# Performance work log

Measured on AMD Instinct MI355X. Metric: run time of the kernel, lower is better.

Reference implementation:

```python
import jax, jax.numpy as jnp
import numpy as np

BLOCK = 64  # bnb 4-bit quant block size along the input dim

def dequant4bit(q, scale):
    # q: [out, in] int codes in [0,16); scale: [out, in//BLOCK]
    # symmetric 4-bit dequant: w = (code - 7.5) * blockwise scale
    return (q.astype(jnp.float32) - 7.5) * jnp.repeat(scale, BLOCK, axis=1)

def setup_inputs() -> dict:
    key = jax.random.key(0)
    ks = jax.random.split(key, 11)
    B, S, D, H, R = 4, 2048, 2048, 8192, 16
    return {
        "x1": jax.random.normal(ks[0], (B, S, D), jnp.float32),
        "w_up_q": jax.random.randint(ks[1], (H, D), 0, 16, dtype=jnp.int32),
        "w_up_scale": jax.random.uniform(ks[2], (H, D // BLOCK), jnp.float32) * 0.02,
        "b_up": jax.random.normal(ks[3], (H,), jnp.float32) * 0.01,
        "w_up_lora_a": jax.random.normal(ks[4], (D, R), jnp.float32) * 0.02,
        "w_up_lora_b": jax.random.normal(ks[5], (R, H), jnp.float32) * 0.02,
        "w_down_q": jax.random.randint(ks[6], (D, H), 0, 16, dtype=jnp.int32),
        "w_down_scale": jax.random.uniform(ks[7], (D, H // BLOCK), jnp.float32) * 0.02,
        "b_down": jax.random.normal(ks[8], (D,), jnp.float32) * 0.01,
        "w_down_lora_a": jax.random.normal(ks[9], (H, R), jnp.float32) * 0.02,
        "w_down_lora_b": jax.random.normal(ks[10], (R, D), jnp.float32) * 0.02,
    }

def reference(x1, w_up_q, w_up_scale, b_up, w_up_lora_a, w_up_lora_b,
              w_down_q, w_down_scale, b_down, w_down_lora_a, w_down_lora_b):
    # up projection: dequant-matmul + bias + LoRA (activation_forward='relu')
    w_up = dequant4bit(w_up_q, w_up_scale).T            # [D, H]
    y1 = x1 @ w_up + b_up + (x1 @ w_up_lora_a) @ w_up_lora_b   # [B, S, H]
    x2 = jax.nn.relu(y1)
    # down projection: dequant-matmul + bias + LoRA
    w_down = dequant4bit(w_down_q, w_down_scale).T      # [H, D]
    y2 = x2 @ w_down + b_down + (x2 @ w_down_lora_a) @ w_down_lora_b  # [B, S, D]
    return y2
```

## Files before the change

### kernel.cpp

```cpp
#include <hip/hip_runtime.h>
#include <hip/hip_bf16.h>
#include <stdint.h>
#include <stddef.h>

typedef __bf16 bf16;
typedef bf16  bf16x4 __attribute__((ext_vector_type(4)));
typedef bf16  bf16x8 __attribute__((ext_vector_type(8)));
typedef float f32x4  __attribute__((ext_vector_type(4)));

__device__ __forceinline__ void async_copy16(bf16* lds, const bf16* g) {
    __builtin_amdgcn_global_load_lds(
        (const __attribute__((address_space(1))) void*)g,
        (__attribute__((address_space(3))) void*)lds,
        16, 0, 0);
}

__device__ __forceinline__ void bar() { __builtin_amdgcn_s_barrier(); }
#define SFENCE() __builtin_amdgcn_sched_barrier(0)
#define WAIT_LGKM0() do { asm volatile("s_waitcnt lgkmcnt(0)"); SFENCE(); } while (0)
#define WAIT_VM6()   do { asm volatile("s_waitcnt vmcnt(6)");   SFENCE(); } while (0)
#define WAIT_VM0()   do { asm volatile("s_waitcnt vmcnt(0)");   SFENCE(); } while (0)

__global__ __launch_bounds__(256) void cast_f32_to_bf16(
        const float* __restrict__ in, bf16* __restrict__ out, int n4) {
    int i = blockIdx.x * blockDim.x + threadIdx.x;
    if (i >= n4) return;
    const float4 v = *(const float4*)(in + (size_t)i * 4);
    bf16x4 o;
    o[0] = (bf16)v.x; o[1] = (bf16)v.y; o[2] = (bf16)v.z; o[3] = (bf16)v.w;
    *(bf16x4*)(out + (size_t)i * 4) = o;
}

__global__ __launch_bounds__(256) void dequant_lora(
        const int*   __restrict__ q,
        const float* __restrict__ scale,
        const float* __restrict__ A,
        const float* __restrict__ Bm,
        bf16* __restrict__ out,
        int N, int K) {
    const int tid = threadIdx.x;
    const int k0 = blockIdx.x * 64;
    const int n0 = blockIdx.y * 64;
    const int kk = k0 + (tid & 15) * 4;
    const int nb = n0 + (tid >> 4) * 4;

    f32x4 Ar[4][4];
    #pragma unroll
    for (int i = 0; i < 4; ++i)
        #pragma unroll
        for (int rq = 0; rq < 4; ++rq)
            Ar[i][rq] = *(const f32x4*)&A[(size_t)(kk + i) * 16 + rq * 4];
    f32x4 Br[16];
    #pragma unroll
    for (int r = 0; r < 16; ++r)
        Br[r] = *(const f32x4*)&Bm[(size_t)r * N + nb];

    const int scol = (unsigned)k0 >> 6;
    #pragma unroll
    for (int nn = 0; nn < 4; ++nn) {
        const int n = nb + nn;
        const int4 qv = *(const int4*)&q[(size_t)n * K + kk];
        const float s = scale[(size_t)n * (K >> 6) + scol];
        float l0 = 0.f, l1 = 0.f, l2 = 0.f, l3 = 0.f;
        #pragma unroll
        for (int r = 0; r < 16; ++r) {
            const float bv = Br[r][nn];
            l0 += Ar[0][r >> 2][r & 3] * bv;
            l1 += Ar[1][r >> 2][r & 3] * bv;
            l2 += Ar[2][r >> 2][r & 3] * bv;
            l3 += Ar[3][r >> 2][r & 3] * bv;
        }
        bf16x4 o;
        o[0] = (bf16)(((float)qv.x - 7.5f) * s + l0);
        o[1] = (bf16)(((float)qv.y - 7.5f) * s + l1);
        o[2] = (bf16)(((float)qv.z - 7.5f) * s + l2);
        o[3] = (bf16)(((float)qv.w - 7.5f) * s + l3);
        *(bf16x4*)&out[(size_t)n * K + kk] = o;
    }
}

template <bool RELU, typename OUT_T>
__global__ __launch_bounds__(512, 2) void gemm_bt256(
        const bf16* __restrict__ A, const bf16* __restrict__ B,
        const float* __restrict__ bias, OUT_T* __restrict__ C,
        int M, int N, int K) {
    __shared__ __attribute__((aligned(16))) bf16 As[2][2][128 * 64];
    __shared__ __attribute__((aligned(16))) bf16 Bs[2][2][128 * 64];

    const int tid  = threadIdx.x;
    const int wave = tid >> 6;
    const int lane = tid & 63;
    const int wm   = wave >> 2;
    const int wn   = wave & 3;
    const int bn   = blockIdx.x;
    const int bm   = blockIdx.y;

    const int srow = tid >> 3;
    const int scol = ((tid & 7) ^ (srow & 7)) * 8;
    const bf16* gA = A + ((size_t)(bm * 256) + srow) * K + scol;
    const bf16* gB = B + ((size_t)(bn * 256) + srow) * K + scol;

    auto STAGE_A = [&](int h, int tt) {
        bf16* l = &As[tt & 1][h][wave * 512];
        const bf16* g = gA + (size_t)h * 128 * K + (size_t)tt * 64;
        async_copy16(l, g);
        async_copy16(l + 4096, g + (size_t)64 * K);
    };
    auto STAGE_B = [&](int h, int tt) {
        bf16* l = &Bs[tt & 1][h][wave * 512];
        const bf16* g = gB + (size_t)h * 128 * K + (size_t)tt * 64;
        async_copy16(l, g);
        async_copy16(l + 4096, g + (size_t)64 * K);
    };

    const int fr  = lane & 15;
    const int kq  = lane >> 4;
    const int cg0 = ((kq    ) ^ (fr & 7)) * 8;
    const int cg1 = ((kq + 4) ^ (fr & 7)) * 8;
    const int ra  = fr * 64;
    const int rb  = (wn & 1) * 4096 + fr * 64;

    f32x4 acc[8][4];
    #pragma unroll
    for (int i = 0; i < 8; ++i)
        #pragma unroll
        for (int j = 0; j < 4; ++j) {
            f32x4 z = {0.f, 0.f, 0.f, 0.f};
            acc[i][j] = z;
        }

    STAGE_B(0, 0); STAGE_B(1, 0); STAGE_A(0, 0); STAGE_A(1, 0);
    STAGE_B(0, 1); STAGE_B(1, 1); STAGE_A(0, 1);
    WAIT_VM6();
    bar();

    const int NT = K >> 6;
    bf16x8 fa[4][2], fb[4][2];

    for (int t = 0; t < NT; ++t) {
        const int p = t & 1;
        const bf16* aH = &As[p][wm][0];
        const bf16* bH = &Bs[p][wn >> 1][0];

        #pragma unroll
        for (int i = 0; i < 4; ++i) {
            fa[i][0] = *(const bf16x8*)(aH + i * 1024 + ra + cg0);
            fa[i][1] = *(const bf16x8*)(aH + i * 1024 + ra + cg1);
        }
        #pragma unroll
        for (int j = 0; j < 4; ++j) {
            fb[j][0] = *(const bf16x8*)(bH + rb + j * 1024 + cg0);
            fb[j][1] = *(const bf16x8*)(bH + rb + j * 1024 + cg1);
        }
        if (t + 1 < NT) STAGE_A(1, t + 1);
        bar();
        WAIT_LGKM0();
        __builtin_amdgcn_s_setprio(1);
        #pragma unroll
        for (int ks = 0; ks < 2; ++ks)
            #pragma unroll
            for (int i = 0; i < 4; ++i)
                #pragma unroll
                for (int j = 0; j < 2; ++j)
                    acc[i][j] = __builtin_amdgcn_mfma_f32_16x16x32_bf16(
                        fa[i][ks], fb[j][ks], acc[i][j], 0, 0, 0);
        __builtin_amdgcn_s_setprio(0);
        bar();

        if (t + 2 < NT) STAGE_B(0, t + 2);
        bar();
        WAIT_LGKM0();
        __builtin_amdgcn_s_setprio(1);
        #pragma unroll
        for (int ks = 0; ks < 2; ++ks)
            #pragma unroll
            for (int i = 0; i < 4; ++i)
                #pragma unroll
                for (int j = 2; j < 4; ++j)
                    acc[i][j] = __builtin_amdgcn_mfma_f32_16x16x32_bf16(
                        fa[i][ks], fb[j][ks], acc[i][j], 0, 0, 0);
        __builtin_amdgcn_s_setprio(0);
        bar();

        #pragma unroll
        for (int i = 0; i < 4; ++i) {
            fa[i][0] = *(const bf16x8*)(aH + (i + 4) * 1024 + ra + cg0);
            fa[i][1] = *(const bf16x8*)(aH + (i + 4) * 1024 + ra + cg1);
        }
        if (t + 2 < NT) STAGE_B(1, t + 2);
        bar();
        WAIT_LGKM0();
        __builtin_amdgcn_s_setprio(1);
        #pragma unroll
        for (int ks = 0; ks < 2; ++ks)
            #pragma unroll
            for (int i = 0; i < 4; ++i)
                #pragma unroll
                for (int j = 2; j < 4; ++j)
                    acc[i + 4][j] = __builtin_amdgcn_mfma_f32_16x16x32_bf16(
                        fa[i][ks], fb[j][ks], acc[i + 4][j], 0, 0, 0);
        __builtin_amdgcn_s_setprio(0);
        bar();

        if (t + 2 < NT) {
            STAGE_A(0, t + 2);
            WAIT_VM6();
        } else {
            WAIT_VM0();
        }
        bar();
        __builtin_amdgcn_s_setprio(1);
        #pragma unroll
        for (int ks = 0; ks < 2; ++ks)
            #pragma unroll
            for (int i = 0; i < 4; ++i)
                #pragma unroll
                for (int j = 0; j < 2; ++j)
                    acc[i + 4][j] = __builtin_amdgcn_mfma_f32_16x16x32_bf16(
                        fa[i][ks], fb[j][ks], acc[i + 4][j], 0, 0, 0);
        __builtin_amdgcn_s_setprio(0);
        bar();
    }

    const int er = bm * 256 + wm * 128 + (lane >> 4) * 4;
    const int ec = bn * 256 + wn * 64 + fr;
    #pragma unroll
    for (int j = 0; j < 4; ++j) {
        const int col = ec + j * 16;
        const float bv = bias[col];
        #pragma unroll
        for (int i = 0; i < 8; ++i) {
            #pragma unroll
            for (int r = 0; r < 4; ++r) {
                const int row = er + i * 16 + r;
                float v = acc[i][j][r] + bv;
                if (RELU) v = v > 0.f ? v : 0.f;
                C[(size_t)row * N + col] = (OUT_T)v;
            }
        }
    }
}

extern "C" void kernel_launch(void* const* d_in, const int* in_sizes, int n_in,
                              void* d_out, int out_size, void* d_ws, size_t ws_size,
                              hipStream_t stream) {
    const float* x1           = (const float*)d_in[0];
    const int*   w_up_q       = (const int*)  d_in[1];
    const float* w_up_scale   = (const float*)d_in[2];
    const float* b_up         = (const float*)d_in[3];
    const float* w_up_lora_a  = (const float*)d_in[4];
    const float* w_up_lora_b  = (const float*)d_in[5];
    const int*   w_down_q     = (const int*)  d_in[6];
    const float* w_down_scale = (const float*)d_in[7];
    const float* b_down       = (const float*)d_in[8];
    const float* w_down_lora_a= (const float*)d_in[9];
    const float* w_down_lora_b= (const float*)d_in[10];
    float* out = (float*)d_out;

    const int M = 8192, D = 2048, H = 8192;

    char* ws = (char*)d_ws;
    bf16* x1b = (bf16*)ws;
    bf16* wup = (bf16*)(ws + (size_t)M * D * 2);
    bf16* x2  = (bf16*)(ws + (size_t)M * D * 2 + (size_t)H * D * 2);
    bf16* wdn = x1b;

    {
        int n4 = (M * D) / 4;
        cast_f32_to_bf16<<<dim3((n4 + 255) / 256), dim3(256), 0, stream>>>(x1, x1b, n4);
    }
    dequant_lora<<<dim3(D / 64, H / 64), dim3(256), 0, stream>>>(
        w_up_q, w_up_scale, w_up_lora_a, w_up_lora_b, wup, H, D);
    gemm_bt256<true, bf16><<<dim3(H / 256, M / 256), dim3(512), 0, stream>>>(
        x1b, wup, b_up, x2, M, H, D);
    dequant_lora<<<dim3(H / 64, D / 64), dim3(256), 0, stream>>>(
        w_down_q, w_down_scale, w_down_lora_a, w_down_lora_b, wdn, D, H);
    gemm_bt256<false, float><<<dim3(D / 256, M / 256), dim3(512), 0, stream>>>(
        x2, wdn, b_down, out, M, D, H);
}
```

Before: 784.3 us.

## Prefetch next A fragments into registers and unroll GEMM loop by two stages

Restructures the 256x256 bf16 GEMM main loop so the first half of the next tile's A fragments is loaded from LDS during the last MFMA phase of the current tile. The loop is unrolled by two, with the LDS buffers split into separate named arrays, so buffer selection is resolved at compile time. LDS waits are moved to after the MFMA blocks instead of before them, overlapping LDS reads with matrix math. This adds another set of fragment registers, which could cause spills at 2 blocks per CU, and assumes NT is even.

```diff
diff --git a/kernel.cpp b/kernel.cpp
--- a/kernel.cpp
+++ b/kernel.cpp
@@ -84,8 +84,10 @@
         const bf16* __restrict__ A, const bf16* __restrict__ B,
         const float* __restrict__ bias, OUT_T* __restrict__ C,
         int M, int N, int K) {
-    __shared__ __attribute__((aligned(16))) bf16 As[2][2][128 * 64];
-    __shared__ __attribute__((aligned(16))) bf16 Bs[2][2][128 * 64];
+    __shared__ __attribute__((aligned(16))) bf16 As0[2][8192];
+    __shared__ __attribute__((aligned(16))) bf16 As1[2][8192];
+    __shared__ __attribute__((aligned(16))) bf16 Bs0[2][8192];
+    __shared__ __attribute__((aligned(16))) bf16 Bs1[2][8192];
 
     const int tid  = threadIdx.x;
     const int wave = tid >> 6;
@@ -100,15 +102,8 @@
     const bf16* gA = A + ((size_t)(bm * 256) + srow) * K + scol;
     const bf16* gB = B + ((size_t)(bn * 256) + srow) * K + scol;
 
-    auto STAGE_A = [&](int h, int tt) {
-        bf16* l = &As[tt & 1][h][wave * 512];
-        const bf16* g = gA + (size_t)h * 128 * K + (size_t)tt * 64;
-        async_copy16(l, g);
-        async_copy16(l + 4096, g + (size_t)64 * K);
-    };
-    auto STAGE_B = [&](int h, int tt) {
-        bf16* l = &Bs[tt & 1][h][wave * 512];
-        const bf16* g = gB + (size_t)h * 128 * K + (size_t)tt * 64;
+    auto stage2 = [&](bf16* halfBase, const bf16* g) {
+        bf16* l = halfBase + wave * 512;
         async_copy16(l, g);
         async_copy16(l + 4096, g + (size_t)64 * K);
     };
@@ -129,97 +124,123 @@
             acc[i][j] = z;
         }
 
-    STAGE_B(0, 0); STAGE_B(1, 0); STAGE_A(0, 0); STAGE_A(1, 0);
-    STAGE_B(0, 1); STAGE_B(1, 1); STAGE_A(0, 1);
+    stage2(&Bs0[0][0], gB);
+    stage2(&Bs0[1][0], gB + (size_t)128 * K);
+    stage2(&As0[0][0], gA);
+    stage2(&As0[1][0], gA + (size_t)128 * K);
+    stage2(&Bs1[0][0], gB + 64);
+    stage2(&Bs1[1][0], gB + (size_t)128 * K + 64);
+    stage2(&As1[0][0], gA + 64);
     WAIT_VM6();
     bar();
 
     const int NT = K >> 6;
-    bf16x8 fa[4][2], fb[4][2];
-
-    for (int t = 0; t < NT; ++t) {
-        const int p = t & 1;
-        const bf16* aH = &As[p][wm][0];
-        const bf16* bH = &Bs[p][wn >> 1][0];
-
+    bf16x8 fan[2][4][2];
+    bf16x8 faB[4][2];
+    bf16x8 fb[4][2];
+
+    {
+        const bf16* aH = &As0[wm][0];
         #pragma unroll
         for (int i = 0; i < 4; ++i) {
-            fa[i][0] = *(const bf16x8*)(aH + i * 1024 + ra + cg0);
-            fa[i][1] = *(const bf16x8*)(aH + i * 1024 + ra + cg1);
-        }
-        #pragma unroll
-        for (int j = 0; j < 4; ++j) {
-            fb[j][0] = *(const bf16x8*)(bH + rb + j * 1024 + cg0);
-            fb[j][1] = *(const bf16x8*)(bH + rb + j * 1024 + cg1);
-        }
-        if (t + 1 < NT) STAGE_A(1, t + 1);
-        bar();
-        WAIT_LGKM0();
-        __builtin_amdgcn_s_setprio(1);
-        #pragma unroll
-        for (int ks = 0; ks < 2; ++ks)
-            #pragma unroll
-            for (int i = 0; i < 4; ++i)
-                #pragma unroll
-                for (int j = 0; j < 2; ++j)
-                    acc[i][j] = __builtin_amdgcn_mfma_f32_16x16x32_bf16(
-                        fa[i][ks], fb[j][ks], acc[i][j], 0, 0, 0);
-        __builtin_amdgcn_s_setprio(0);
-        bar();
-
-        if (t + 2 < NT) STAGE_B(0, t + 2);
-        bar();
-        WAIT_LGKM0();
-        __builtin_amdgcn_s_setprio(1);
-        #pragma unroll
-        for (int ks = 0; ks < 2; ++ks)
-            #pragma unroll
-            for (int i = 0; i < 4; ++i)
-                #pragma unroll
-                for (int j = 2; j < 4; ++j)
-                    acc[i][j] = __builtin_amdgcn_mfma_f32_16x16x32_bf16(
-                        fa[i][ks], fb[j][ks], acc[i][j], 0, 0, 0);
-        __builtin_amdgcn_s_setprio(0);
-        bar();
-
-        #pragma unroll
-        for (int i = 0; i < 4; ++i) {
-            fa[i][0] = *(const bf16x8*)(aH + (i + 4) * 1024 + ra + cg0);
-            fa[i][1] = *(const bf16x8*)(aH + (i + 4) * 1024 + ra + cg1);
-        }
-        if (t + 2 < NT) STAGE_B(1, t + 2);
-        bar();
-        WAIT_LGKM0();
-        __builtin_amdgcn_s_setprio(1);
-        #pragma unroll
-        for (int ks = 0; ks < 2; ++ks)
-            #pragma unroll
-            for (int i = 0; i < 4; ++i)
-                #pragma unroll
-                for (int j = 2; j < 4; ++j)
-                    acc[i + 4][j] = __builtin_amdgcn_mfma_f32_16x16x32_bf16(
-                        fa[i][ks], fb[j][ks], acc[i + 4][j], 0, 0, 0);
-        __builtin_amdgcn_s_setprio(0);
-        bar();
-
-        if (t + 2 < NT) {
-            STAGE_A(0, t + 2);
-            WAIT_VM6();
-        } else {
-            WAIT_VM0();
-        }
-        bar();
-        __builtin_amdgcn_s_setprio(1);
-        #pragma unroll
-        for (int ks = 0; ks < 2; ++ks)
-            #pragma unroll
-            for (int i = 0; i < 4; ++i)
-                #pragma unroll
-                for (int j = 0; j < 2; ++j)
-                    acc[i + 4][j] = __builtin_amdgcn_mfma_f32_16x16x32_bf16(
-                        fa[i][ks], fb[j][ks], acc[i + 4][j], 0, 0, 0);
-        __builtin_amdgcn_s_setprio(0);
-        bar();
+            fan[0][i][0] = *(const bf16x8*)(aH + i * 1024 + ra + cg0);
+            fan[0][i][1] = *(const bf16x8*)(aH + i * 1024 + ra + cg1);
+        }
+    }
+
+    for (int t0 = 0; t0 < NT; t0 += 2) {
+        #pragma unroll
+        for (int u = 0; u < 2; ++u) {
+            const int t = t0 + u;
+            bf16 (*AsC)[8192] = u ? As1 : As0;
+            bf16 (*AsN)[8192] = u ? As0 : As1;
+            bf16 (*BsC)[8192] = u ? Bs1 : Bs0;
+            const bf16* aC = &AsC[wm][0];
+            const bf16* bC = &BsC[wn >> 1][0];
+            const bf16* aN = &AsN[wm][0];
+
+            #pragma unroll
+            for (int j = 0; j < 4; ++j) {
+                fb[j][0] = *(const bf16x8*)(bC + rb + j * 1024 + cg0);
+                fb[j][1] = *(const bf16x8*)(bC + rb + j * 1024 + cg1);
+            }
+            if (t + 1 < NT)
+                stage2(&AsN[1][0], gA + (size_t)128 * K + (size_t)(t + 1) * 64);
+            bar();
+            __builtin_amdgcn_s_setprio(1);
+            #pragma unroll
+            for (int ks = 0; ks < 2; ++ks)
+                #pragma unroll
+                for (int i = 0; i < 4; ++i)
+                    #pragma unroll
+                    for (int j = 0; j < 2; ++j)
+                        acc[i][j] = __builtin_amdgcn_mfma_f32_16x16x32_bf16(
+                            fan[u][i][ks], fb[j][ks], acc[i][j], 0, 0, 0);
+            __builtin_amdgcn_s_setprio(0);
+            WAIT_LGKM0();
+            bar();
+
+            #pragma unroll
+            for (int i = 0; i < 4; ++i) {
+                faB[i][0] = *(const bf16x8*)(aC + (i + 4) * 1024 + ra + cg0);
+                faB[i][1] = *(const bf16x8*)(aC + (i + 4) * 1024 + ra + cg1);
+            }
+            if (t + 2 < NT)
+                stage2(&BsC[0][0], gB + (size_t)(t + 2) * 64);
+            bar();
+            __builtin_amdgcn_s_setprio(1);
+            #pragma unroll
+            for (int ks = 0; ks < 2; ++ks)
+                #pragma unroll
+                for (int i = 0; i < 4; ++i)
+                    #pragma unroll
+                    for (int j = 2; j < 4; ++j)
+                        acc[i][j] = __builtin_amdgcn_mfma_f32_16x16x32_bf16(
+                            fan[u][i][ks], fb[j][ks], acc[i][j], 0, 0, 0);
+            __builtin_amdgcn_s_setprio(0);
+            bar();
+
+            if (t + 2 < NT)
+                stage2(&BsC[1][0], gB + (size_t)128 * K + (size_t)(t + 2) * 64);
+            bar();
+            __builtin_amdgcn_s_setprio(1);
+            #pragma unroll
+            for (int ks = 0; ks < 2; ++ks)
+                #pragma unroll
+                for (int i = 0; i < 4; ++i)
+                    #pragma unroll
+                    for (int j = 2; j < 4; ++j)
+                        acc[i + 4][j] = __builtin_amdgcn_mfma_f32_16x16x32_bf16(
+                            faB[i][ks], fb[j][ks], acc[i + 4][j], 0, 0, 0);
+            __builtin_amdgcn_s_setprio(0);
+            bar();
+
+            if (t + 2 < NT) {
+                stage2(&AsC[0][0], gA + (size_t)(t + 2) * 64);
+                WAIT_VM6();
+            } else {
+                WAIT_VM0();
+            }
+            bar();
+            if (t + 1 < NT) {
+                #pragma unroll
+                for (int i = 0; i < 4; ++i) {
+                    fan[u ^ 1][i][0] = *(const bf16x8*)(aN + i * 1024 + ra + cg0);
+                    fan[u ^ 1][i][1] = *(const bf16x8*)(aN + i * 1024 + ra + cg1);
+                }
+            }
+            __builtin_amdgcn_s_setprio(1);
+            #pragma unroll
+            for (int ks = 0; ks < 2; ++ks)
+                #pragma unroll
+                for (int i = 0; i < 4; ++i)
+                    #pragma unroll
+                    for (int j = 0; j < 2; ++j)
+                        acc[i + 4][j] = __builtin_amdgcn_mfma_f32_16x16x32_bf16(
+                            faB[i][ks], fb[j][ks], acc[i + 4][j], 0, 0, 0);
+            __builtin_amdgcn_s_setprio(0);
+            bar();
+        }
     }
 
     const int er = bm * 256 + wm * 128 + (lane >> 4) * 4;
```

New measurement: 2.365 ms. 202% more time.
